# Kernel tuning notes

Hardware: AMD Instinct MI355X
Metric: run time of the kernel (lower is better)

## Reference

```python
import jax, jax.numpy as jnp
import numpy as np

G, P, F, K = 256, 512, 4, 6   # graphs, nodes/graph, features, knn k
N = G * P

def _prelu(x, a):
    return jnp.where(x >= 0, x, a * x)

def _knn_edges(x):
    # per-graph brute-force kNN (k=6, no self loops), flow source->target
    xg = x.reshape(G, P, F)
    sq = jnp.sum(xg * xg, -1)                                   # [G,P]
    d = sq[:, :, None] + sq[:, None, :] - 2.0 * jnp.einsum('gpf,gqf->gpq', xg, xg)
    d = d + jnp.eye(P, dtype=x.dtype) * 1e10                    # exclude self
    _, idx = jax.lax.top_k(-d, K)                               # [G,P,K] neighbors
    off = (jnp.arange(G) * P)[:, None, None]
    src = (idx + off).reshape(-1)                               # message sources
    tgt = jnp.broadcast_to(jnp.arange(N).reshape(G, P, 1), (G, P, K)).reshape(-1)
    return src, tgt

def setup_inputs():
    key = jax.random.key(0)
    ks = jax.random.split(key, 8)
    f = lambda k, s: jax.random.normal(k, s, jnp.float32) * 0.1
    return {
        "x": jax.random.normal(ks[0], (N, F), jnp.float32),
        "batch": jnp.arange(N, dtype=jnp.int32) // P,
        "pre_W1": f(ks[1], (F, F)), "pre_b1": jnp.zeros((F,), jnp.float32),
        "pre_a1": jnp.full((F,), 0.25, jnp.float32),
        "pre_W2": f(ks[2], (F, F)), "pre_b2": jnp.zeros((F,), jnp.float32),
        "pre_a2": jnp.full((F,), 0.25, jnp.float32),
        "bn_g": jnp.ones((F,), jnp.float32), "bn_b": jnp.zeros((F,), jnp.float32),
        "act_a": jnp.full((F,), 0.25, jnp.float32),
        "conv_Wm": f(ks[3], (4, F, F)), "conv_bm": jnp.zeros((4, F), jnp.float32),
        "hlv_W1": f(ks[4], (5 * F, 5 * F)), "hlv_b1": jnp.zeros((5 * F,), jnp.float32),
        "hlv_W2": f(ks[5], (5 * F, 1)), "hlv_b2": jnp.zeros((1,), jnp.float32),
    }

def reference(x, batch, pre_W1, pre_b1, pre_a1, pre_W2, pre_b2, pre_a2,
              bn_g, bn_b, act_a, conv_Wm, conv_bm, hlv_W1, hlv_b1, hlv_W2, hlv_b2):
    src, tgt = _knn_edges(x)                                    # knn on raw x
    # pre_nn: Linear-PReLU-Linear-PReLU-BatchNorm (batch stats, training mode)
    h = _prelu(x @ pre_W1 + pre_b1, pre_a1)
    h = _prelu(h @ pre_W2 + pre_b2, pre_a2)
    mu = jnp.mean(h, 0)
    var = jnp.var(h, 0)
    h = (h - mu) / jnp.sqrt(var + 1e-5) * bn_g + bn_b
    xs = [h]
    for i in range(4):
        # GeneralConv (PyG defaults): sum-aggregate lin_msg(x_j) + identity skip
        msg = h[src] @ conv_Wm[i] + conv_bm[i]                  # [E,F]
        aggr = jax.ops.segment_sum(msg, tgt, num_segments=N)    # [N,F]
        h = _prelu(aggr + h, act_a)                             # shared PReLU act
        xs.append(h)
    hc = jnp.concatenate(xs, axis=-1)                           # JK 'cat' -> [N,5F]
    pooled = jax.ops.segment_sum(hc, batch, num_segments=G)     # global_add_pool
    out = jax.nn.relu(pooled @ hlv_W1 + hlv_b1) @ hlv_W2 + hlv_b2
    return out
```

## Files before the change

### kernel.cpp

```cpp
#include <hip/hip_runtime.h>

#define GG 256
#define PP 512
#define FF 4
#define KK 6
#define NN (GG*PP)

__device__ __forceinline__ float finf(){ return __int_as_float(0x7f800000); }

__device__ __forceinline__ void cas6_u64(uint64_t (&B)[6], uint64_t kv)
{
    bool c1 = kv < B[1]; bool c2 = kv < B[2]; bool c3 = kv < B[3];
    bool c4 = kv < B[4]; bool c5 = kv < B[5];
    B[0] = c1 ? B[1] : kv;
    B[1] = c2 ? B[2] : (c1 ? kv : B[1]);
    B[2] = c3 ? B[3] : (c2 ? kv : B[2]);
    B[3] = c4 ? B[4] : (c3 ? kv : B[3]);
    B[4] = c5 ? B[5] : (c4 ? kv : B[4]);
    B[5] = c5 ? kv : B[5];
}

__global__ __launch_bounds__(512) void scan_kernel(
    const float* __restrict__ x,
    const float* __restrict__ pre_W1, const float* __restrict__ pre_b1, const float* __restrict__ pre_a1,
    const float* __restrict__ pre_W2, const float* __restrict__ pre_b2, const float* __restrict__ pre_a2,
    float* __restrict__ bn_part,
    int* __restrict__ knn_idx)
{
    __shared__ float4   xm2s[PP];
    __shared__ float    sqs[PP];
    __shared__ float    lists[128][29];
    __shared__ float    Tv[128];
    __shared__ unsigned cnt[128];
    __shared__ float    wred[8][8];

    const int t = threadIdx.x;
    const int bid = blockIdx.x;
    const int g = bid >> 2, quarter = bid & 3;
    const int gbase = g * PP;
    const int w = t >> 6, lane = t & 63;
    const int s  = w & 3;
    const int lt = (w >> 2)*64 + lane;
    const int p  = quarter*128 + lt;

    float4 xt = ((const float4*)x)[gbase + t];
    xm2s[t] = make_float4(-2.0f*xt.x, -2.0f*xt.y, -2.0f*xt.z, -2.0f*xt.w);
    sqs[t]  = xt.x*xt.x + xt.y*xt.y + xt.z*xt.z + xt.w*xt.w;

    if (quarter == 0){
        float h1[FF], h2[FF];
#pragma unroll
        for (int fo=0;fo<FF;fo++){
            float m = xt.x*pre_W1[0*FF+fo] + xt.y*pre_W1[1*FF+fo]
                    + xt.z*pre_W1[2*FF+fo] + xt.w*pre_W1[3*FF+fo] + pre_b1[fo];
            h1[fo] = m >= 0.0f ? m : pre_a1[fo]*m;
        }
#pragma unroll
        for (int fo=0;fo<FF;fo++){
            float m = h1[0]*pre_W2[0*FF+fo] + h1[1]*pre_W2[1*FF+fo]
                    + h1[2]*pre_W2[2*FF+fo] + h1[3]*pre_W2[3*FF+fo] + pre_b2[fo];
            h2[fo] = m >= 0.0f ? m : pre_a2[fo]*m;
        }
        float v[8];
#pragma unroll
        for (int f=0;f<4;f++){ v[f]=h2[f]; v[4+f]=h2[f]*h2[f]; }
#pragma unroll
        for (int off=32; off; off>>=1){
#pragma unroll
            for (int f=0;f<8;f++) v[f] += __shfl_down(v[f], off);
        }
        if ((t&63)==0){
#pragma unroll
            for (int f=0;f<8;f++) wred[w][f]=v[f];
        }
    }
    __syncthreads();
    if (quarter == 0 && t < 8){
        float a=0;
#pragma unroll
        for (int w2=0;w2<8;w2++) a += wred[w2][t];
        bn_part[t*GG + g] = a;
    }

    const int su = __builtin_amdgcn_readfirstlane(s);
    const int qb = su*128;

    float4 xm = xm2s[p];
    float4 xp = make_float4(-0.5f*xm.x, -0.5f*xm.y, -0.5f*xm.z, -0.5f*xm.w);

    const float INF = finf();
    float A0=INF,A1=INF,A2=INF,A3=INF,A4=INF,A5=INF,A6=INF;
    uint64_t mask = 0;

#pragma unroll 16
    for (int j=0;j<64;j++){
        float4 a = xm2s[qb + 2*j];
        float4 b = xm2s[qb + 2*j + 1];
        float da = fmaf(a.x,xp.x, fmaf(a.y,xp.y, fmaf(a.z,xp.z, fmaf(a.w,xp.w, sqs[qb+2*j]))));
        float db = fmaf(b.x,xp.x, fmaf(b.y,xp.y, fmaf(b.z,xp.z, fmaf(b.w,xp.w, sqs[qb+2*j+1]))));
        float b0 = fminf(da,db), b1 = fmaxf(da,db);
        mask = (mask << 1) | (uint64_t)(b0 <= A6 ? 1u : 0u);
        float x0=fmaxf(A0,b0), x1=fmaxf(A1,b0), x2=fmaxf(A2,b0),
              x3=fmaxf(A3,b0), x4=fmaxf(A4,b0), x5=fmaxf(A5,b0);
        float y0=fmaxf(A0,b1), y1=fmaxf(A1,b1), y2=fmaxf(A2,b1),
              y3=fmaxf(A3,b1), y4=fmaxf(A4,b1);
        float C0 = fminf(A0, b0);
        float C1 = fminf(fminf(A1, x0), b1);
        float C2 = fminf(fminf(A2, x1), y0);
        float C3 = fminf(fminf(A3, x2), y1);
        float C4 = fminf(fminf(A4, x3), y2);
        float C5 = fminf(fminf(A5, x4), y3);
        float C6 = fminf(fminf(A6, x5), y4);
        A0=C0; A1=C1; A2=C2; A3=C3; A4=C4; A5=C5; A6=C6;
    }

    lists[lt][s*7+0]=A0; lists[lt][s*7+1]=A1; lists[lt][s*7+2]=A2;
    lists[lt][s*7+3]=A3; lists[lt][s*7+4]=A4; lists[lt][s*7+5]=A5;
    lists[lt][s*7+6]=A6;
    __syncthreads();

    if (t < 128){
        float M0=INF,M1=INF,M2=INF,M3=INF,M4=INF,M5=INF,M6=INF;
#pragma unroll
        for (int j=0;j<28;j++){
            float v = lists[t][j];
            float n0=fminf(M0,v);
            float n1=fminf(M1,fmaxf(v,M0));
            float n2=fminf(M2,fmaxf(v,M1));
            float n3=fminf(M3,fmaxf(v,M2));
            float n4=fminf(M4,fmaxf(v,M3));
            float n5=fminf(M5,fmaxf(v,M4));
            float n6=fminf(M6,fmaxf(v,M5));
            M0=n0;M1=n1;M2=n2;M3=n3;M4=n4;M5=n5;M6=n6;
        }
        Tv[t] = M6;
        cnt[t] = 0;
    }
    __syncthreads();

    {
        const float T = Tv[lt];
        uint64_t m = mask;
        while (__ballot(m != 0)){
            if (m){
                int k = __builtin_ctzll(m);
                m &= m - 1;
                int pj = 63 - k;
                int q0 = qb + 2*pj;
                float4 a = xm2s[q0];
                float4 b = xm2s[q0+1];
                float da = fmaf(a.x,xp.x, fmaf(a.y,xp.y, fmaf(a.z,xp.z, fmaf(a.w,xp.w, sqs[q0]))));
                float db = fmaf(b.x,xp.x, fmaf(b.y,xp.y, fmaf(b.z,xp.z, fmaf(b.w,xp.w, sqs[q0+1]))));
                if (da <= T && q0 != p){
                    unsigned jj = atomicAdd(&cnt[lt], 1u);
                    if (jj < 6) knn_idx[jj*NN + gbase + p] = q0;
                }
                if (db <= T && (q0+1) != p){
                    unsigned jj = atomicAdd(&cnt[lt], 1u);
                    if (jj < 6) knn_idx[jj*NN + gbase + p] = q0 + 1;
                }
            }
        }
    }
    __syncthreads();

    if (t < 128 && cnt[t] > 6){
        const int pt = quarter*128 + t;
        float4 xmq = xm2s[pt];
        float4 xq = make_float4(-0.5f*xmq.x, -0.5f*xmq.y, -0.5f*xmq.z, -0.5f*xmq.w);
        uint64_t B[6];
#pragma unroll
        for (int j=0;j<6;j++) B[j] = ~0ull;
        for (int q=0;q<PP;q++){
            if (q == pt) continue;
            float4 a = xm2s[q];
            float d = fmaf(a.x,xq.x, fmaf(a.y,xq.y, fmaf(a.z,xq.z, fmaf(a.w,xq.w, sqs[q]))));
            int bb = __float_as_int(d);
            unsigned uu = (bb >= 0) ? ((unsigned)bb ^ 0x80000000u) : (unsigned)(~bb);
            uint64_t key = ((uint64_t)uu << 32) | (unsigned)q;
            if (key < B[0]) cas6_u64(B, key);
        }
#pragma unroll
        for (int j=0;j<6;j++)
            knn_idx[j*NN + gbase + pt] = (int)(B[j] & 0xFFFFFFFFull);
    }
}

__global__ __launch_bounds__(512) void graph_kernel(
    const float* __restrict__ x,
    const int* __restrict__ knn_idx,
    const float* __restrict__ bn_part,
    const float* __restrict__ pre_W1, const float* __restrict__ pre_b1, const float* __restrict__ pre_a1,
    const float* __restrict__ pre_W2, const float* __restrict__ pre_b2, const float* __restrict__ pre_a2,
    const float* __restrict__ bn_g, const float* __restrict__ bn_b,
    const float* __restrict__ act_a,
    const float* __restrict__ conv_Wm, const float* __restrict__ conv_bm,
    const float* __restrict__ hlv_W1, const float* __restrict__ hlv_b1,
    const float* __restrict__ hlv_W2, const float* __restrict__ hlv_b2,
    float* __restrict__ out)
{
    __shared__ float4 hbuf[PP];
    __shared__ float wred[8][4];
    __shared__ float pooled[20];
    __shared__ float stats[8];
    __shared__ float hid[20];
    const int g = blockIdx.x, p = threadIdx.x;
    const int gp = g*PP + p;

    if (p < 64){
        int vv = p>>3, j = p&7;
        float acc = 0.0f;
        for (int i=j;i<GG;i+=8) acc += bn_part[vv*GG + i];
        acc += __shfl_xor(acc,1); acc += __shfl_xor(acc,2); acc += __shfl_xor(acc,4);
        if (j==0) stats[vv] = acc;
    }
    __syncthreads();
    if (p < 4){
        float mu  = stats[p]   * (1.0f/NN);
        float var = stats[4+p] * (1.0f/NN) - mu*mu;
        stats[p]   = mu;
        stats[4+p] = 1.0f / sqrtf(var + 1e-5f);
    }

    float4 xt = ((const float4*)x)[gp];
    float h1[FF], h2[FF];
#pragma unroll
    for (int fo=0;fo<FF;fo++){
        float m = xt.x*pre_W1[0*FF+fo] + xt.y*pre_W1[1*FF+fo]
                + xt.z*pre_W1[2*FF+fo] + xt.w*pre_W1[3*FF+fo] + pre_b1[fo];
        h1[fo] = m >= 0.0f ? m : pre_a1[fo]*m;
    }
#pragma unroll
    for (int fo=0;fo<FF;fo++){
        float m = h1[0]*pre_W2[0*FF+fo] + h1[1]*pre_W2[1*FF+fo]
                + h1[2]*pre_W2[2*FF+fo] + h1[3]*pre_W2[3*FF+fo] + pre_b2[fo];
        h2[fo] = m >= 0.0f ? m : pre_a2[fo]*m;
    }
    __syncthreads();

    float hp[4];
#pragma unroll
    for (int f=0;f<4;f++)
        hp[f] = (h2[f] - stats[f]) * stats[4+f] * bn_g[f] + bn_b[f];
    hbuf[p] = make_float4(hp[0],hp[1],hp[2],hp[3]);
    int nb[KK];
#pragma unroll
    for (int j=0;j<KK;j++) nb[j] = knn_idx[j*NN + gp];

    auto block_accum = [&](const float* h, int slice){
        float v0=h[0], v1=h[1], v2=h[2], v3=h[3];
#pragma unroll
        for (int off=32; off; off>>=1){
            v0 += __shfl_down(v0,off); v1 += __shfl_down(v1,off);
            v2 += __shfl_down(v2,off); v3 += __shfl_down(v3,off);
        }
        int w = p>>6;
        if ((p&63)==0){ wred[w][0]=v0; wred[w][1]=v1; wred[w][2]=v2; wred[w][3]=v3; }
        __syncthreads();
        if (p < 4){
            float a=0;
#pragma unroll
            for (int w2=0;w2<8;w2++) a += wred[w2][p];
            pooled[slice*4+p] = a;
        }
        __syncthreads();
    };

    block_accum(hp, 0);

#pragma unroll 1
    for (int L=0; L<4; L++){
        float4 sm = make_float4(0.f,0.f,0.f,0.f);
#pragma unroll
        for (int j=0;j<KK;j++){
            float4 hn = hbuf[nb[j]];
            sm.x+=hn.x; sm.y+=hn.y; sm.z+=hn.z; sm.w+=hn.w;
        }
        const float* W  = conv_Wm + L*16;
        const float* bm = conv_bm + L*4;
        float nh[4];
#pragma unroll
        for (int fo=0;fo<4;fo++){
            float m = sm.x*W[0*4+fo] + sm.y*W[1*4+fo] + sm.z*W[2*4+fo] + sm.w*W[3*4+fo]
                    + 6.0f*bm[fo] + hp[fo];
            float a = act_a[fo];
            nh[fo] = m >= 0.0f ? m : a*m;
        }
        __syncthreads();
        hbuf[p] = make_float4(nh[0],nh[1],nh[2],nh[3]);
#pragma unroll
        for (int f=0;f<4;f++) hp[f]=nh[f];
        block_accum(hp, L+1);
    }

    if (p < 20){
        float acc = hlv_b1[p];
#pragma unroll 1
        for (int k2=0;k2<20;k2++) acc += pooled[k2]*hlv_W1[k2*20+p];
        hid[p] = acc > 0.0f ? acc : 0.0f;
    }
    __syncthreads();
    if (p == 0){
        float o = hlv_b2[0];
#pragma unroll 1
        for (int j=0;j<20;j++) o += hid[j]*hlv_W2[j];
        out[g] = o;
    }
}

extern "C" void kernel_launch(void* const* d_in, const int* in_sizes, int n_in,
                              void* d_out, int out_size, void* d_ws, size_t ws_size,
                              hipStream_t stream)
{
    const float* x      = (const float*)d_in[0];
    const float* pre_W1 = (const float*)d_in[2];
    const float* pre_b1 = (const float*)d_in[3];
    const float* pre_a1 = (const float*)d_in[4];
    const float* pre_W2 = (const float*)d_in[5];
    const float* pre_b2 = (const float*)d_in[6];
    const float* pre_a2 = (const float*)d_in[7];
    const float* bn_g   = (const float*)d_in[8];
    const float* bn_b   = (const float*)d_in[9];
    const float* act_a  = (const float*)d_in[10];
    const float* conv_Wm= (const float*)d_in[11];
    const float* conv_bm= (const float*)d_in[12];
    const float* hlv_W1 = (const float*)d_in[13];
    const float* hlv_b1 = (const float*)d_in[14];
    const float* hlv_W2 = (const float*)d_in[15];
    const float* hlv_b2 = (const float*)d_in[16];

    char* ws = (char*)d_ws;
    int*   knn     = (int*)ws;
    float* bn_part = (float*)(ws + (size_t)6*NN*sizeof(int));

    scan_kernel<<<GG*4, PP, 0, stream>>>(x, pre_W1,pre_b1,pre_a1,
                                         pre_W2,pre_b2,pre_a2, bn_part, knn);
    graph_kernel<<<GG, PP, 0, stream>>>(x, knn, bn_part,
                                        pre_W1,pre_b1,pre_a1, pre_W2,pre_b2,pre_a2,
                                        bn_g,bn_b, act_a, conv_Wm,conv_bm,
                                        hlv_W1,hlv_b1,hlv_W2,hlv_b2,
                                        (float*)d_out);
}
```

Baseline: 63.88 us.

## Replace per-candidate top-7 network with group-min threshold and hit-list refinement

The first pass no longer keeps a running 7-element sorted list per thread. Each thread now takes the minimum distance over groups of 16 candidates and quantises it to a rounded-up 16-bit key. Those keys are merged into a conservative 7th-smallest threshold. A second full pass collects the indices under the threshold into a small shared hit list, and one thread per point does an exact top-6 over those hits. A brute-force 512-candidate fallback runs only when a hit list overflows. This removes many min/max ops per candidate and the atomics and ballot loop, in exchange for a second distance pass and a looser threshold that can produce more hits.

```diff
diff --git a/kernel.cpp b/kernel.cpp
--- a/kernel.cpp
+++ b/kernel.cpp
@@ -6,7 +6,15 @@
 #define KK 6
 #define NN (GG*PP)
 
+__device__ __forceinline__ unsigned umin_(unsigned a, unsigned b){ return a<b?a:b; }
+__device__ __forceinline__ unsigned umax_(unsigned a, unsigned b){ return a>b?a:b; }
 __device__ __forceinline__ float finf(){ return __int_as_float(0x7f800000); }
+
+__device__ __forceinline__ unsigned mmap32(float d){
+    int bb = __float_as_int(d);
+    int t = bb >> 31;
+    return (unsigned)(bb ^ (t | (int)0x80000000));
+}
 
 __device__ __forceinline__ void cas6_u64(uint64_t (&B)[6], uint64_t kv)
 {
@@ -20,6 +28,16 @@
     B[5] = c5 ? kv : B[5];
 }
 
+#define INS7U(v){                                  \
+    unsigned n0=umin_(M0,(v));                     \
+    unsigned n1=umin_(M1,umax_((v),M0));           \
+    unsigned n2=umin_(M2,umax_((v),M1));           \
+    unsigned n3=umin_(M3,umax_((v),M2));           \
+    unsigned n4=umin_(M4,umax_((v),M3));           \
+    unsigned n5=umin_(M5,umax_((v),M4));           \
+    unsigned n6=umin_(M6,umax_((v),M5));           \
+    M0=n0;M1=n1;M2=n2;M3=n3;M4=n4;M5=n5;M6=n6; }
+
 __global__ __launch_bounds__(512) void scan_kernel(
     const float* __restrict__ x,
     const float* __restrict__ pre_W1, const float* __restrict__ pre_b1, const float* __restrict__ pre_a1,
@@ -29,9 +47,10 @@
 {
     __shared__ float4   xm2s[PP];
     __shared__ float    sqs[PP];
-    __shared__ float    lists[128][29];
+    __shared__ unsigned gmp[128][17];
     __shared__ float    Tv[128];
-    __shared__ unsigned cnt[128];
+    __shared__ ushort   hits[128*50];
+    __shared__ unsigned cnt4[128][4];
     __shared__ float    wred[8][8];
 
     const int t = threadIdx.x;
@@ -85,104 +104,106 @@
     const int su = __builtin_amdgcn_readfirstlane(s);
     const int qb = su*128;
 
-    float4 xm = xm2s[p];
-    float4 xp = make_float4(-0.5f*xm.x, -0.5f*xm.y, -0.5f*xm.z, -0.5f*xm.w);
-
+    const float4 xmv = xm2s[p];
+    const float4 xp = make_float4(-0.5f*xmv.x, -0.5f*xmv.y, -0.5f*xmv.z, -0.5f*xmv.w);
     const float INF = finf();
-    float A0=INF,A1=INF,A2=INF,A3=INF,A4=INF,A5=INF,A6=INF;
-    uint64_t mask = 0;
-
-#pragma unroll 16
-    for (int j=0;j<64;j++){
-        float4 a = xm2s[qb + 2*j];
-        float4 b = xm2s[qb + 2*j + 1];
-        float da = fmaf(a.x,xp.x, fmaf(a.y,xp.y, fmaf(a.z,xp.z, fmaf(a.w,xp.w, sqs[qb+2*j]))));
-        float db = fmaf(b.x,xp.x, fmaf(b.y,xp.y, fmaf(b.z,xp.z, fmaf(b.w,xp.w, sqs[qb+2*j+1]))));
-        float b0 = fminf(da,db), b1 = fmaxf(da,db);
-        mask = (mask << 1) | (uint64_t)(b0 <= A6 ? 1u : 0u);
-        float x0=fmaxf(A0,b0), x1=fmaxf(A1,b0), x2=fmaxf(A2,b0),
-              x3=fmaxf(A3,b0), x4=fmaxf(A4,b0), x5=fmaxf(A5,b0);
-        float y0=fmaxf(A0,b1), y1=fmaxf(A1,b1), y2=fmaxf(A2,b1),
-              y3=fmaxf(A3,b1), y4=fmaxf(A4,b1);
-        float C0 = fminf(A0, b0);
-        float C1 = fminf(fminf(A1, x0), b1);
-        float C2 = fminf(fminf(A2, x1), y0);
-        float C3 = fminf(fminf(A3, x2), y1);
-        float C4 = fminf(fminf(A4, x3), y2);
-        float C5 = fminf(fminf(A5, x4), y3);
-        float C6 = fminf(fminf(A6, x5), y4);
-        A0=C0; A1=C1; A2=C2; A3=C3; A4=C4; A5=C5; A6=C6;
-    }
-
-    lists[lt][s*7+0]=A0; lists[lt][s*7+1]=A1; lists[lt][s*7+2]=A2;
-    lists[lt][s*7+3]=A3; lists[lt][s*7+4]=A4; lists[lt][s*7+5]=A5;
-    lists[lt][s*7+6]=A6;
+
+#pragma unroll 1
+    for (int gp2=0; gp2<4; gp2++){
+        unsigned packed = 0;
+#pragma unroll
+        for (int sub=0; sub<2; sub++){
+            const int base = qb + (gp2*2+sub)*16;
+            float gm = INF;
+#pragma unroll
+            for (int pj=0; pj<8; pj++){
+                const int q0 = base + pj*2;
+                float4 a = xm2s[q0], b = xm2s[q0+1];
+                float2 sq = *(const float2*)&sqs[q0];
+                float da = fmaf(a.x,xp.x, fmaf(a.y,xp.y, fmaf(a.z,xp.z, fmaf(a.w,xp.w, sq.x))));
+                float db = fmaf(b.x,xp.x, fmaf(b.y,xp.y, fmaf(b.z,xp.z, fmaf(b.w,xp.w, sq.y))));
+                gm = fminf(gm, fminf(da, db));
+            }
+            unsigned u = mmap32(gm);
+            unsigned r = (u >> 16) + ((u & 0xFFFFu) ? 1u : 0u);
+            r = umin_(r, 0xFFFFu);
+            packed |= r << (16*sub);
+        }
+        gmp[lt][su*4 + gp2] = packed;
+    }
     __syncthreads();
 
     if (t < 128){
-        float M0=INF,M1=INF,M2=INF,M3=INF,M4=INF,M5=INF,M6=INF;
-#pragma unroll
-        for (int j=0;j<28;j++){
-            float v = lists[t][j];
-            float n0=fminf(M0,v);
-            float n1=fminf(M1,fmaxf(v,M0));
-            float n2=fminf(M2,fmaxf(v,M1));
-            float n3=fminf(M3,fmaxf(v,M2));
-            float n4=fminf(M4,fmaxf(v,M3));
-            float n5=fminf(M5,fmaxf(v,M4));
-            float n6=fminf(M6,fmaxf(v,M5));
-            M0=n0;M1=n1;M2=n2;M3=n3;M4=n4;M5=n5;M6=n6;
-        }
-        Tv[t] = M6;
-        cnt[t] = 0;
+        unsigned M0=~0u,M1=~0u,M2=~0u,M3=~0u,M4=~0u,M5=~0u,M6=~0u;
+#pragma unroll
+        for (int j=0;j<16;j++){
+            unsigned pr = gmp[t][j];
+            unsigned v0 = pr & 0xFFFFu, v1 = pr >> 16;
+            INS7U(v0); INS7U(v1);
+        }
+        unsigned Tcmp = M6 << 16;
+        Tv[t] = (Tcmp & 0x80000000u) ? __uint_as_float(Tcmp ^ 0x80000000u)
+                                     : __uint_as_float(~Tcmp);
     }
     __syncthreads();
 
     {
-        const float T = Tv[lt];
-        uint64_t m = mask;
-        while (__ballot(m != 0)){
-            if (m){
-                int k = __builtin_ctzll(m);
-                m &= m - 1;
-                int pj = 63 - k;
-                int q0 = qb + 2*pj;
-                float4 a = xm2s[q0];
-                float4 b = xm2s[q0+1];
-                float da = fmaf(a.x,xp.x, fmaf(a.y,xp.y, fmaf(a.z,xp.z, fmaf(a.w,xp.w, sqs[q0]))));
-                float db = fmaf(b.x,xp.x, fmaf(b.y,xp.y, fmaf(b.z,xp.z, fmaf(b.w,xp.w, sqs[q0+1]))));
-                if (da <= T && q0 != p){
-                    unsigned jj = atomicAdd(&cnt[lt], 1u);
-                    if (jj < 6) knn_idx[jj*NN + gbase + p] = q0;
-                }
-                if (db <= T && (q0+1) != p){
-                    unsigned jj = atomicAdd(&cnt[lt], 1u);
-                    if (jj < 6) knn_idx[jj*NN + gbase + p] = q0 + 1;
-                }
+        const float Tf = Tv[lt];
+        unsigned c = 0;
+        ushort* hrow = &hits[lt*50 + su*12];
+#pragma unroll 2
+        for (int j=0;j<64;j++){
+            const int q0 = qb + 2*j;
+            float4 a = xm2s[q0], b = xm2s[q0+1];
+            float2 sq = *(const float2*)&sqs[q0];
+            float da = fmaf(a.x,xp.x, fmaf(a.y,xp.y, fmaf(a.z,xp.z, fmaf(a.w,xp.w, sq.x))));
+            float db = fmaf(b.x,xp.x, fmaf(b.y,xp.y, fmaf(b.z,xp.z, fmaf(b.w,xp.w, sq.y))));
+            bool hA = (da <= Tf), hB = (db <= Tf);
+            if (hA || hB){
+                int i0 = hA ? q0 : (q0+1);
+                hrow[umin_(c,11u)] = (ushort)i0; c++;
+                if (hA && hB){ hrow[umin_(c,11u)] = (ushort)(q0+1); c++; }
             }
         }
-    }
-    __syncthreads();
-
-    if (t < 128 && cnt[t] > 6){
+        cnt4[lt][su] = c;
+    }
+    __syncthreads();
+
+    if (t < 128){
+        uint4 cc = *(const uint4*)&cnt4[t][0];
         const int pt = quarter*128 + t;
+        bool ovf = (cc.x>12u)||(cc.y>12u)||(cc.z>12u)||(cc.w>12u);
         float4 xmq = xm2s[pt];
         float4 xq = make_float4(-0.5f*xmq.x, -0.5f*xmq.y, -0.5f*xmq.z, -0.5f*xmq.w);
         uint64_t B[6];
 #pragma unroll
-        for (int j=0;j<6;j++) B[j] = ~0ull;
-        for (int q=0;q<PP;q++){
-            if (q == pt) continue;
-            float4 a = xm2s[q];
-            float d = fmaf(a.x,xq.x, fmaf(a.y,xq.y, fmaf(a.z,xq.z, fmaf(a.w,xq.w, sqs[q]))));
-            int bb = __float_as_int(d);
-            unsigned uu = (bb >= 0) ? ((unsigned)bb ^ 0x80000000u) : (unsigned)(~bb);
-            uint64_t key = ((uint64_t)uu << 32) | (unsigned)q;
-            if (key < B[0]) cas6_u64(B, key);
-        }
-#pragma unroll
-        for (int j=0;j<6;j++)
-            knn_idx[j*NN + gbase + pt] = (int)(B[j] & 0xFFFFFFFFull);
+        for (int j2=0;j2<6;j2++) B[j2] = ~0ull;
+        if (!ovf){
+#pragma unroll
+            for (int s2=0;s2<4;s2++){
+                unsigned cs = (s2==0)?cc.x:(s2==1)?cc.y:(s2==2)?cc.z:cc.w;
+                const ushort* hr = &hits[t*50 + s2*12];
+                for (unsigned j2=0;j2<cs;j2++){
+                    int idx = hr[j2];
+                    float4 a = xm2s[idx];
+                    float d = fmaf(a.x,xq.x, fmaf(a.y,xq.y, fmaf(a.z,xq.z, fmaf(a.w,xq.w, sqs[idx]))));
+                    uint64_t key = ((uint64_t)mmap32(d) << 32) | (unsigned)idx;
+                    if (idx == pt) key = ~0ull;
+                    if (key < B[0]) cas6_u64(B, key);
+                }
+            }
+        } else {
+            for (int q=0;q<PP;q++){
+                float4 a = xm2s[q];
+                float d = fmaf(a.x,xq.x, fmaf(a.y,xq.y, fmaf(a.z,xq.z, fmaf(a.w,xq.w, sqs[q]))));
+                uint64_t key = ((uint64_t)mmap32(d) << 32) | (unsigned)q;
+                if (q == pt) key = ~0ull;
+                if (key < B[0]) cas6_u64(B, key);
+            }
+        }
+#pragma unroll
+        for (int j2=0;j2<6;j2++)
+            knn_idx[j2*NN + gbase + pt] = (int)(B[j2] & 0xFFFFFFFFull);
     }
 }
 
```

After: 64.51 us. No clear change (+1.0%).
